# Optimization experiments

Hardware: AMD Instinct MI355X
Metric: run time of the kernel (lower is better)

## Reference

```python
import jax, jax.numpy as jnp
import numpy as np

NB, NA, NEI = 16, 1024, 64            # batch, atoms per system, neighbors per atom
NTYPE, NWAVE, NIPSIN = 4, 8, 3        # element types, radial waves, angular order (s,p,d)
CUTOFF = 6.0
P = NA * NEI                          # pairs per batch element
LEN_IDX = sum(3 ** i for i in range(NIPSIN))  # 1 + 3 + 9 = 13
INDEX_PARA = np.concatenate([np.full(3 ** i, i) for i in range(NIPSIN)])  # (13,)


def setup_inputs() -> dict:
    key = jax.random.key(0)
    ks = jax.random.split(key, 7)
    coordinates = jax.random.normal(ks[0], (NB, NA, 3), jnp.float32)
    numatoms = jnp.full((NB, 1), NA, dtype=jnp.int32)
    atom_index = jax.random.randint(ks[1], (NB, 2, P), 0, NA, dtype=jnp.int32)
    shifts = jax.random.normal(ks[2], (NB, P, 3), jnp.float32) * 0.01  # small PBC-like shifts, all valid
    species = jax.random.randint(ks[3], (NB * NA,), 0, NTYPE, dtype=jnp.int32)
    rs = jax.random.uniform(ks[4], (NTYPE, NWAVE), jnp.float32, 0.0, CUTOFF)
    inta = jax.random.uniform(ks[5], (NTYPE, NWAVE), jnp.float32, 0.5, 1.5)
    params = jax.random.uniform(ks[6], (NTYPE,), jnp.float32, 0.5, 1.5)
    return dict(coordinates=coordinates, numatoms=numatoms, atom_index=atom_index,
                shifts=shifts, species=species, rs=rs, inta=inta, params=params)


def _density_forward(coordinates, atom_index, shifts, species, rs, inta, params):
    totnatom = NB * NA
    # (nb, 2, P) -> (2, nb*P) global flattened atom indices
    idx = jnp.transpose(atom_index, (1, 0, 2)).reshape(2, -1)
    offs = jnp.repeat(jnp.arange(NB, dtype=idx.dtype) * NA, P)
    idx12 = idx + offs[None, :]                          # (2, M)
    shifts_f = shifts.reshape(-1, 3)                     # (M, 3)
    valid = jnp.all(shifts_f > -1e9, axis=-1)            # padding mask (faithful to torch nonzero filter)

    cart = coordinates.reshape(-1, 3)[idx12]             # (2, M, 3) gather
    dist_vec = cart[0] - cart[1] + shifts_f              # (M, 3)
    dist = jnp.linalg.norm(dist_vec, axis=-1)            # (M,)
    dist_safe = jnp.where(dist > 1e-12, dist, 1.0)

    # cutoff_cosine, zeroed for padded pairs (every angular term carries f_cut)
    f_cut = 0.5 * (jnp.cos(jnp.pi * jnp.minimum(dist / CUTOFF, 1.0)) + 1.0)
    f_cut = jnp.where(valid, f_cut, 0.0)

    nb_spec = species[idx12[0]]                          # (M,) neighbor i-atom type
    # gaussian radial basis, per-type params gathered instead of type loop
    radial = jnp.exp(-inta[nb_spec] * jnp.square(dist[:, None] - rs[nb_spec]))  # (M, NWAVE)

    # angular: iterated outer products of the unit distance vector, seeded by f_cut
    unit = dist_vec / dist_safe[:, None]                 # (M, 3)
    feats = [f_cut[:, None]]
    orb = f_cut[:, None]
    for _ in range(1, NIPSIN):
        orb = (orb[:, :, None] * unit[:, None, :]).reshape(orb.shape[0], -1)
        feats.append(orb)
    angular = jnp.concatenate(feats, axis=1)             # (M, 13)

    orbital = angular[:, :, None] * radial[:, None, :]   # (M, 13, NWAVE)

    # scatter-add per (center atom, neighbor type) in one fused segment_sum
    seg = idx12[0] * NTYPE + nb_spec
    acc = jax.ops.segment_sum(orbital, seg, num_segments=totnatom * NTYPE)
    acc = acc.reshape(totnatom, NTYPE, LEN_IDX, NWAVE)

    sq = jnp.square(acc)
    # sum angular components belonging to the same l (index_para groups)
    onehot = jax.nn.one_hot(jnp.asarray(INDEX_PARA), NIPSIN, dtype=sq.dtype)  # (13, NIPSIN)
    dens = jnp.einsum('ntkw,kl->ntlw', sq, onehot)       # (N, NTYPE, NIPSIN, NWAVE)
    density = dens.reshape(totnatom, NTYPE, NIPSIN * NWAVE)

    d = density * params[None, :, None]                  # einsum('ijk,j->ijk')
    # sqrt(einsum('ilj,imj->ijlm')).flatten(2,3).sum(-1)
    out = jnp.sqrt(d[:, :, None, :] * d[:, None, :, :]).sum(axis=(1, 2))  # (N, NIPSIN*NWAVE)
    return out


def reference(coordinates, numatoms, atom_index, shifts, species, rs, inta, params):
    del numatoms  # unused by the original forward math
    return _density_forward(coordinates, atom_index, shifts, species, rs, inta, params)
```

## Files before the change

### kernel.cpp

```cpp
#include <hip/hip_runtime.h>
#include <hip/hip_fp16.h>
#include <math.h>

namespace {
constexpr int kNB  = 16;
constexpr int kNA  = 1024;
constexpr int kP   = 65536;
constexpr int kNW  = 8;
constexpr int kTot = kNB * kNA;
constexpr int kMaxNei = 128;
constexpr float kInvCut = 1.0f / 6.0f;
constexpr float kPi = 3.14159265358979323846f;

constexpr int kChunkPairs = 4096;
constexpr int kBuildThreads = 1024;
constexpr int kPerThread = kChunkPairs / kBuildThreads;
}

__global__ __launch_bounds__(kBuildThreads) void build_lists(
    const float* __restrict__ coords,
    const int*   __restrict__ aidx,
    const float* __restrict__ shifts,
    int*   __restrict__ cnt,
    uint4* __restrict__ lists)
{
  __shared__ int hist[kNA];

  const int tid = threadIdx.x;
  const int r = blockIdx.x & 7;
  const int q = blockIdx.x >> 3;
  const int b = r + ((q >> 4) << 3);
  const int chunk = q & 15;
  const int pairBase = chunk * kChunkPairs;

  if (tid < kNA) hist[tid] = 0;
  __syncthreads();

  uint4    pay[kPerThread];
  unsigned meta[kPerThread];

#pragma unroll
  for (int it = 0; it < kPerThread; ++it) {
    const int p = pairBase + it * kBuildThreads + tid;

    const int i0 = __builtin_nontemporal_load(&aidx[(b * 2 + 0) * kP + p]);
    const int i1 = __builtin_nontemporal_load(&aidx[(b * 2 + 1) * kP + p]);
    const int gi = b * kNA + i0;
    const int gj = b * kNA + i1;

    const size_t sb = (size_t)(b * kP + p) * 3;
    const float sx = __builtin_nontemporal_load(&shifts[sb + 0]);
    const float sy = __builtin_nontemporal_load(&shifts[sb + 1]);
    const float sz = __builtin_nontemporal_load(&shifts[sb + 2]);
    const bool valid = (sx > -1.0e9f) & (sy > -1.0e9f) & (sz > -1.0e9f);

    const float dx = coords[gi * 3 + 0] - coords[gj * 3 + 0] + sx;
    const float dy = coords[gi * 3 + 1] - coords[gj * 3 + 1] + sy;
    const float dz = coords[gi * 3 + 2] - coords[gj * 3 + 2] + sz;

    const float dist = sqrtf(dx * dx + dy * dy + dz * dz);
    const float rr = dist * kInvCut;
    float f = 0.5f * (__cosf(kPi * fminf(rr, 1.0f)) + 1.0f);
    if (!valid | (rr >= 1.0f)) f = 0.0f;

    unsigned m = 0u;
    if (f != 0.0f) {
      const int rank = atomicAdd(&hist[i0], 1);
      m = 0x80000000u | ((unsigned)rank << 10) | (unsigned)i0;
      const float inv = (dist > 1e-12f) ? (1.0f / dist) : 1.0f;
      const float ux = dx * inv, uy = dy * inv, uz = dz * inv;
      pay[it].x = __builtin_bit_cast(unsigned, dist);
      pay[it].y = __builtin_bit_cast(unsigned, f);
      pay[it].z = __builtin_bit_cast(unsigned, __floats2half2_rn(ux, uy));
      pay[it].w = __builtin_bit_cast(unsigned, __floats2half2_rn(uz, 0.0f));
    }
    meta[it] = m;
  }
  __syncthreads();

  if (tid < kNA) {
    const int c = hist[tid];
    int base = 0;
    if (c > 0) base = atomicAdd(&cnt[b * kNA + tid], c);
    hist[tid] = base;
  }
  __syncthreads();

#pragma unroll
  for (int it = 0; it < kPerThread; ++it) {
    const unsigned m = meta[it];
    if (m & 0x80000000u) {
      const int lid  = (int)(m & 1023u);
      const int rank = (int)((m >> 10) & 0xFFFu);
      const int pos  = hist[lid] + rank;
      if (pos < kMaxNei) {
        lists[(size_t)(b * kNA + lid) * kMaxNei + pos] = pay[it];
      }
    }
  }
}

__global__ __launch_bounds__(256) void gather_density(
    const uint4* __restrict__ lists,
    const int*   __restrict__ cnt,
    const int*   __restrict__ species,
    const float* __restrict__ rs,
    const float* __restrict__ inta,
    const float* __restrict__ params,
    float* __restrict__ out)
{
  const int r = blockIdx.x & 7;
  const int m = blockIdx.x >> 3;
  const int b = r + ((m >> 7) << 3);
  const int g = m & 127;
  const int i = b * kNA + g * 8 + (threadIdx.x >> 5);
  const int k = (threadIdx.x >> 3) & 3;
  const int w = threadIdx.x & 7;

  const int s = species[i];
  const float rsw   = rs[s * kNW + w];
  const float intaw = inta[s * kNW + w];
  const int n = min(cnt[i], kMaxNei);
  const int Q = (n + 3) >> 2;
  const int j0 = k * Q;
  const uint4* __restrict__ L = lists + (size_t)i * kMaxNei;

  float a[13];
#pragma unroll
  for (int mm = 0; mm < 13; ++mm) a[mm] = 0.0f;

#pragma unroll 4
  for (int t = 0; t < Q; ++t) {
    const int j = j0 + t;
    const uint4 u = L[j];
    if (j < n) {
      const float dist = __builtin_bit_cast(float, u.x);
      const float f    = __builtin_bit_cast(float, u.y);
      const float2 uxy = __half22float2(__builtin_bit_cast(__half2, u.z));
      const float2 uzp = __half22float2(__builtin_bit_cast(__half2, u.w));
      const float ux = uxy.x, uy = uxy.y, uz = uzp.x;
      const float dr = dist - rsw;
      const float rad = __expf(-intaw * dr * dr);
      const float fr = f * rad;
      a[0] += fr;
      const float rx = fr * ux, ry = fr * uy, rz = fr * uz;
      a[1] += rx;        a[2] += ry;        a[3] += rz;
      a[4] += rx * ux;   a[5] += rx * uy;   a[6] += rx * uz;
      a[7] += ry * ux;   a[8] += ry * uy;   a[9] += ry * uz;
      a[10] += rz * ux;  a[11] += rz * uy;  a[12] += rz * uz;
    }
  }

#pragma unroll
  for (int mm = 0; mm < 13; ++mm) {
    a[mm] += __shfl_xor(a[mm], 8);
    a[mm] += __shfl_xor(a[mm], 16);
  }

  if (k == 0) {
    const float pm = params[s];
    const float o0 = a[0] * a[0];
    const float o1 = a[1] * a[1] + a[2] * a[2] + a[3] * a[3];
    const float o2 = a[4] * a[4] + a[5] * a[5] + a[6] * a[6] +
                     a[7] * a[7] + a[8] * a[8] + a[9] * a[9] +
                     a[10] * a[10] + a[11] * a[11] + a[12] * a[12];
    float* o = out + (size_t)i * 24;
    o[0 * kNW + w] = pm * o0;
    o[1 * kNW + w] = pm * o1;
    o[2 * kNW + w] = pm * o2;
  }
}

extern "C" void kernel_launch(void* const* d_in, const int* in_sizes, int n_in,
                              void* d_out, int out_size, void* d_ws, size_t ws_size,
                              hipStream_t stream) {
  const float* coords  = (const float*)d_in[0];
  const int*   aidx    = (const int*)d_in[2];
  const float* shifts  = (const float*)d_in[3];
  const int*   species = (const int*)d_in[4];
  const float* rs      = (const float*)d_in[5];
  const float* inta    = (const float*)d_in[6];
  const float* params  = (const float*)d_in[7];
  float* out = (float*)d_out;

  int*   cnt   = (int*)d_ws;
  uint4* lists = (uint4*)((char*)d_ws + (size_t)kTot * sizeof(int));

  hipMemsetAsync(cnt, 0, (size_t)kTot * sizeof(int), stream);

  const int nchunks = (kNB * kP) / kChunkPairs;
  build_lists<<<nchunks, kBuildThreads, 0, stream>>>(coords, aidx, shifts,
                                                     cnt, lists);
  gather_density<<<(kTot * 32) / 256, 256, 0, stream>>>(lists, cnt, species,
                                                        rs, inta, params, out);
}
```

Baseline: 105.3 us.

## Stage build_lists output in LDS sorted by atom before writing lists

Adds a block-wide prefix scan over the per-atom histogram so each pair can be placed into a shared-memory staging buffer grouped by center atom. Threads then write the staged entries to the global neighbor lists in sorted order, so consecutive threads write to consecutive slots of the same atom's list. This replaces scattered 16-byte stores, which are meant to be the main write cost. In exchange it adds a 64 KB LDS buffer, an extra scan, more barriers, and packs the atom id into the unused half of the payload's w word.

Measured after the change: 105.9 us. No clear change (+0.6%).

```diff
diff --git a/kernel.cpp b/kernel.cpp
--- a/kernel.cpp
+++ b/kernel.cpp
@@ -12,9 +12,10 @@
 constexpr float kInvCut = 1.0f / 6.0f;
 constexpr float kPi = 3.14159265358979323846f;
 
-constexpr int kChunkPairs = 4096;
 constexpr int kBuildThreads = 1024;
-constexpr int kPerThread = kChunkPairs / kBuildThreads;
+constexpr int kPerThread = 4;
+constexpr int kChunkPairs = kBuildThreads * kPerThread;
+constexpr int kChunksPerB = kP / kChunkPairs;
 }
 
 __global__ __launch_bounds__(kBuildThreads) void build_lists(
@@ -24,16 +25,20 @@
     int*   __restrict__ cnt,
     uint4* __restrict__ lists)
 {
-  __shared__ int hist[kNA];
+  __shared__ int   hist[kNA];
+  __shared__ int   ofs[kNA];
+  __shared__ int   wsum[16];
+  __shared__ int   totalS;
+  __shared__ uint4 stage[kChunkPairs];
 
   const int tid = threadIdx.x;
   const int r = blockIdx.x & 7;
   const int q = blockIdx.x >> 3;
   const int b = r + ((q >> 4) << 3);
-  const int chunk = q & 15;
+  const int chunk = q & (kChunksPerB - 1);
   const int pairBase = chunk * kChunkPairs;
 
-  if (tid < kNA) hist[tid] = 0;
+  hist[tid] = 0;
   __syncthreads();
 
   uint4    pay[kPerThread];
@@ -78,12 +83,34 @@
   }
   __syncthreads();
 
-  if (tid < kNA) {
-    const int c = hist[tid];
-    int base = 0;
-    if (c > 0) base = atomicAdd(&cnt[b * kNA + tid], c);
-    hist[tid] = base;
-  }
+  const int lane = tid & 63;
+  const int wv   = tid >> 6;
+  const int selfc = hist[tid];
+  int val = selfc;
+#pragma unroll
+  for (int o = 1; o < 64; o <<= 1) {
+    const int t = __shfl_up(val, o);
+    if (lane >= o) val += t;
+  }
+  if (lane == 63) wsum[wv] = val;
+  __syncthreads();
+  if (wv == 0) {
+    int wval = (lane < 16) ? wsum[lane] : 0;
+#pragma unroll
+    for (int o = 1; o < 16; o <<= 1) {
+      const int t = __shfl_up(wval, o);
+      if (lane >= o) wval += t;
+    }
+    if (lane < 16) wsum[lane] = wval;
+    if (lane == 15) totalS = wval;
+  }
+  __syncthreads();
+  const int wbase = (wv == 0) ? 0 : wsum[wv - 1];
+  ofs[tid] = wbase + val - selfc;
+
+  int base = 0;
+  if (selfc > 0) base = atomicAdd(&cnt[b * kNA + tid], selfc);
+  hist[tid] = base;
   __syncthreads();
 
 #pragma unroll
@@ -92,10 +119,21 @@
     if (m & 0x80000000u) {
       const int lid  = (int)(m & 1023u);
       const int rank = (int)((m >> 10) & 0xFFFu);
-      const int pos  = hist[lid] + rank;
-      if (pos < kMaxNei) {
-        lists[(size_t)(b * kNA + lid) * kMaxNei + pos] = pay[it];
-      }
+      uint4 u = pay[it];
+      u.w = (u.w & 0xFFFFu) | ((unsigned)lid << 16);
+      stage[ofs[lid] + rank] = u;
+    }
+  }
+  __syncthreads();
+
+  const int T = totalS;
+  for (int t = tid; t < T; t += kBuildThreads) {
+    const uint4 u = stage[t];
+    const int a    = (int)(u.w >> 16);
+    const int rank = t - ofs[a];
+    const int pos  = hist[a] + rank;
+    if (pos < kMaxNei) {
+      lists[(size_t)(b * kNA + a) * kMaxNei + pos] = u;
     }
   }
 }
@@ -188,8 +226,8 @@
 
   hipMemsetAsync(cnt, 0, (size_t)kTot * sizeof(int), stream);
 
-  const int nchunks = (kNB * kP) / kChunkPairs;
-  build_lists<<<nchunks, kBuildThreads, 0, stream>>>(coords, aidx, shifts,
+  const int nblocks = kNB * kChunksPerB;
+  build_lists<<<nblocks, kBuildThreads, 0, stream>>>(coords, aidx, shifts,
                                                      cnt, lists);
   gather_density<<<(kTot * 32) / 256, 256, 0, stream>>>(lists, cnt, species,
                                                         rs, inta, params, out);
```
